# Kernel optimization log

Measured on AMD Instinct MI355X. Metric: run time of the kernel, lower is better.

## Reference

```python
import jax, jax.numpy as jnp
import numpy as np

TEMPERATURE = 8.0  # sqrt(head_dim=64)
NEG_INF = -1.0e9


def setup_inputs() -> dict:
    key = jax.random.key(0)
    kq, kk, kv, ks, km = jax.random.split(key, 5)
    B, H, S, D = 4, 8, 1024, 64
    q = jax.random.normal(kq, (B, H, S, D), dtype=jnp.float32)
    k = jax.random.normal(kk, (B, H, S, D), dtype=jnp.float32)
    v = jax.random.normal(kv, (B, H, S, D), dtype=jnp.float32)
    sph = jax.random.uniform(ks, (B, H, S, S), dtype=jnp.float32)
    mask = jax.random.randint(km, (B, 1, S, S), 0, 2, dtype=jnp.int32)
    return {"q": q, "k": k, "v": v, "sph": sph, "mask": mask}


def reference(q, k, v, sph, mask):
    # scores: [B,H,S,S]
    attn = jnp.einsum("bhqd,bhkd->bhqk", q / TEMPERATURE, k)
    attn = attn * sph
    attn = jnp.where(mask == 0, NEG_INF, attn)
    p_attn = jax.nn.softmax(attn, axis=-1)  # dropout in eval mode = identity
    output = jnp.einsum("bhqk,bhkd->bhqd", p_attn, v)
    return (output, p_attn)
```

## Files before the change

kernel.cpp:

```cpp
#include <hip/hip_runtime.h>

#define S_DIM 1024
#define D_DIM 64
#define TQ 16

typedef __attribute__((ext_vector_type(4))) float f32x4;
typedef __attribute__((ext_vector_type(4))) int i32x4;
typedef __attribute__((ext_vector_type(4))) unsigned short u16x4;
typedef __attribute__((ext_vector_type(8))) short short8;

__device__ inline unsigned short f2bf(float x) {
  unsigned int u = __builtin_bit_cast(unsigned int, x);
  u += 0x7fffu + ((u >> 16) & 1u);
  return (unsigned short)(u >> 16);
}

__device__ inline short8 pack8(f32x4 a, f32x4 b) {
  short8 r;
  r[0] = (short)f2bf(a.x); r[1] = (short)f2bf(a.y);
  r[2] = (short)f2bf(a.z); r[3] = (short)f2bf(a.w);
  r[4] = (short)f2bf(b.x); r[5] = (short)f2bf(b.y);
  r[6] = (short)f2bf(b.z); r[7] = (short)f2bf(b.w);
  return r;
}

__global__ __launch_bounds__(256, 3)
void sdpa_kernel(const float* __restrict__ qp, const float* __restrict__ kp,
                 const float* __restrict__ vp, const float* __restrict__ sphp,
                 const int* __restrict__ maskp,
                 float* __restrict__ outp, float* __restrict__ pp)
{
  __shared__ unsigned short pb[TQ][1032];
  __shared__ unsigned short vt[64][136];
  __shared__ float          red[2][4][16];

  const int tid   = threadIdx.x;
  const int lane  = tid & 63;
  const int wave  = tid >> 6;
  const int row16 = lane & 15;
  const int quad  = lane >> 4;

  const int bh = blockIdx.x >> 6;
  const int qt = blockIdx.x & 63;
  const int b  = bh >> 3;
  const int q0 = qt * TQ;

  const size_t bhS = (size_t)bh * S_DIM;

  const float* qrow = qp + (bhS + q0 + row16) * D_DIM + quad * 8;
  const f32x4 s8 = {0.125f, 0.125f, 0.125f, 0.125f};
  f32x4 qa = *(const f32x4*)(qrow);
  f32x4 qb = *(const f32x4*)(qrow + 4);
  f32x4 qc = *(const f32x4*)(qrow + 32);
  f32x4 qd = *(const f32x4*)(qrow + 36);
  const short8 bq0 = pack8(qa * s8, qb * s8);
  const short8 bq1 = pack8(qc * s8, qd * s8);

  const int kbase = wave * 256;
  f32x4 accs[16];
  #pragma unroll
  for (int t = 0; t < 16; ++t) {
    const float* krow = kp + (bhS + kbase + t * 16 + row16) * D_DIM + quad * 8;
    f32x4 ka = *(const f32x4*)(krow);
    f32x4 kb = *(const f32x4*)(krow + 4);
    f32x4 kc = *(const f32x4*)(krow + 32);
    f32x4 kd = *(const f32x4*)(krow + 36);
    f32x4 acc = {0.f, 0.f, 0.f, 0.f};
    acc = __builtin_amdgcn_mfma_f32_16x16x32_bf16(pack8(ka, kb), bq0, acc, 0, 0, 0);
    acc = __builtin_amdgcn_mfma_f32_16x16x32_bf16(pack8(kc, kd), bq1, acc, 0, 0, 0);
    accs[t] = acc;
  }

  const int q = q0 + row16;
  const float* sprow = sphp + (bhS + q) * S_DIM + kbase + quad * 4;
  const int*   mrow  = maskp + ((size_t)b * S_DIM + q) * S_DIM + kbase + quad * 4;

  float mx = -3.0e38f;
  #pragma unroll
  for (int t = 0; t < 16; ++t) {
    f32x4 p4 = *(const f32x4*)(sprow + t * 16);
    i32x4 m4 = *(const i32x4*)(mrow + t * 16);
    f32x4 s  = accs[t];
    s.x = (m4.x == 0) ? -1.0e9f : s.x * p4.x;
    s.y = (m4.y == 0) ? -1.0e9f : s.y * p4.y;
    s.z = (m4.z == 0) ? -1.0e9f : s.z * p4.z;
    s.w = (m4.w == 0) ? -1.0e9f : s.w * p4.w;
    accs[t] = s;
    mx = fmaxf(mx, fmaxf(fmaxf(s.x, s.y), fmaxf(s.z, s.w)));
  }
  mx = fmaxf(mx, __shfl_xor(mx, 16));
  mx = fmaxf(mx, __shfl_xor(mx, 32));
  if (quad == 0) red[0][wave][row16] = mx;
  __syncthreads();
  mx = fmaxf(fmaxf(red[0][0][row16], red[0][1][row16]),
             fmaxf(red[0][2][row16], red[0][3][row16]));

  float sum = 0.f;
  #pragma unroll
  for (int t = 0; t < 16; ++t) {
    f32x4 e;
    e.x = __expf(accs[t].x - mx);
    e.y = __expf(accs[t].y - mx);
    e.z = __expf(accs[t].z - mx);
    e.w = __expf(accs[t].w - mx);
    accs[t] = e;
    sum += (e.x + e.y) + (e.z + e.w);
  }
  sum += __shfl_xor(sum, 16);
  sum += __shfl_xor(sum, 32);
  if (quad == 0) red[1][wave][row16] = sum;
  __syncthreads();
  sum = (red[1][0][row16] + red[1][1][row16]) + (red[1][2][row16] + red[1][3][row16]);
  const float inv = 1.0f / sum;

  float* prow = pp + (bhS + q) * S_DIM + kbase + quad * 4;
  #pragma unroll
  for (int t = 0; t < 16; ++t) {
    f32x4 pv = accs[t] * inv;
    *(f32x4*)(prow + t * 16) = pv;
    u16x4 pbv;
    pbv.x = f2bf(pv.x); pbv.y = f2bf(pv.y);
    pbv.z = f2bf(pv.z); pbv.w = f2bf(pv.w);
    *(u16x4*)&pb[row16][kbase + t * 16 + quad * 4] = pbv;
  }

  f32x4 oacc = {0.f, 0.f, 0.f, 0.f};
  const float* vbase = vp + bhS * D_DIM;
  for (int vc = 0; vc < 8; ++vc) {
    __syncthreads();
    #pragma unroll
    for (int it = 0; it < 8; ++it) {
      const int i  = it * 256 + tid;
      const int c4 = i >> 7, rr = i & 127;
      f32x4 vv = *(const f32x4*)(vbase + (size_t)(vc * 128 + rr) * D_DIM + c4 * 4);
      vt[c4 * 4 + 0][rr] = f2bf(vv.x);
      vt[c4 * 4 + 1][rr] = f2bf(vv.y);
      vt[c4 * 4 + 2][rr] = f2bf(vv.z);
      vt[c4 * 4 + 3][rr] = f2bf(vv.w);
    }
    __syncthreads();
    #pragma unroll
    for (int kk = 0; kk < 4; ++kk) {
      short8 af = *(const short8*)&vt[wave * 16 + row16][kk * 32 + quad * 8];
      short8 bf = *(const short8*)&pb[row16][vc * 128 + kk * 32 + quad * 8];
      oacc = __builtin_amdgcn_mfma_f32_16x16x32_bf16(af, bf, oacc, 0, 0, 0);
    }
  }

  float* orow = outp + (bhS + q0 + row16) * D_DIM + wave * 16 + quad * 4;
  *(f32x4*)orow = oacc;
}

extern "C" void kernel_launch(void* const* d_in, const int* in_sizes, int n_in,
                              void* d_out, int out_size, void* d_ws, size_t ws_size,
                              hipStream_t stream) {
  const float* q    = (const float*)d_in[0];
  const float* k    = (const float*)d_in[1];
  const float* v    = (const float*)d_in[2];
  const float* sph  = (const float*)d_in[3];
  const int*   mask = (const int*)d_in[4];
  float* out  = (float*)d_out;
  float* patt = out + (size_t)4 * 8 * 1024 * 64;

  dim3 grid(32 * 64);
  dim3 block(256);
  hipLaunchKernelGGL(sdpa_kernel, grid, block, 0, stream,
                     q, k, v, sph, mask, out, patt);
}
```

Before: 390.9 us.

## Switch to fp16 MFMA and row-wise coalesced sph/mask/P access via LDS staging

Scores are staged in LDS as fp16 instead of being kept in registers, so each wave processes whole rows with contiguous 1 KB loads of sph and mask and contiguous stores of P. Previously each lane read and wrote 16-byte pieces strided across the key axis. Normalisation of the output is deferred to the end, and bf16 is replaced by fp16 with a -60000 mask sentinel. The main cost targeted is the poor coalescing of the large sph, mask and P streams. In exchange the kernel does extra LDS round trips and shuffle reductions per row, and fp16 storage of unnormalised scores loses some precision.

```diff
diff --git a/kernel.cpp b/kernel.cpp
--- a/kernel.cpp
+++ b/kernel.cpp
@@ -1,26 +1,19 @@
 #include <hip/hip_runtime.h>
 
 #define S_DIM 1024
-#define D_DIM 64
 #define TQ 16
 
 typedef __attribute__((ext_vector_type(4))) float f32x4;
 typedef __attribute__((ext_vector_type(4))) int i32x4;
-typedef __attribute__((ext_vector_type(4))) unsigned short u16x4;
-typedef __attribute__((ext_vector_type(8))) short short8;
+typedef _Float16 half4 __attribute__((ext_vector_type(4)));
+typedef _Float16 half8 __attribute__((ext_vector_type(8)));
 
-__device__ inline unsigned short f2bf(float x) {
-  unsigned int u = __builtin_bit_cast(unsigned int, x);
-  u += 0x7fffu + ((u >> 16) & 1u);
-  return (unsigned short)(u >> 16);
-}
-
-__device__ inline short8 pack8(f32x4 a, f32x4 b) {
-  short8 r;
-  r[0] = (short)f2bf(a.x); r[1] = (short)f2bf(a.y);
-  r[2] = (short)f2bf(a.z); r[3] = (short)f2bf(a.w);
-  r[4] = (short)f2bf(b.x); r[5] = (short)f2bf(b.y);
-  r[6] = (short)f2bf(b.z); r[7] = (short)f2bf(b.w);
+__device__ inline half8 pack8h(f32x4 a, f32x4 b) {
+  half8 r;
+  r[0] = (_Float16)a.x; r[1] = (_Float16)a.y;
+  r[2] = (_Float16)a.z; r[3] = (_Float16)a.w;
+  r[4] = (_Float16)b.x; r[5] = (_Float16)b.y;
+  r[6] = (_Float16)b.z; r[7] = (_Float16)b.w;
   return r;
 }
 
@@ -30,9 +23,9 @@
                  const int* __restrict__ maskp,
                  float* __restrict__ outp, float* __restrict__ pp)
 {
-  __shared__ unsigned short pb[TQ][1032];
-  __shared__ unsigned short vt[64][136];
-  __shared__ float          red[2][4][16];
+  __shared__ _Float16 pb[TQ][1032];
+  __shared__ _Float16 vt[64][136];
+  __shared__ float    red[2][4][16];
 
   const int tid   = threadIdx.x;
   const int lane  = tid & 63;
@@ -47,108 +40,116 @@
 
   const size_t bhS = (size_t)bh * S_DIM;
 
-  const float* qrow = qp + (bhS + q0 + row16) * D_DIM + quad * 8;
+  const float* qrow = qp + (bhS + q0 + row16) * 64 + quad * 8;
   const f32x4 s8 = {0.125f, 0.125f, 0.125f, 0.125f};
   f32x4 qa = *(const f32x4*)(qrow);
   f32x4 qb = *(const f32x4*)(qrow + 4);
   f32x4 qc = *(const f32x4*)(qrow + 32);
   f32x4 qd = *(const f32x4*)(qrow + 36);
-  const short8 bq0 = pack8(qa * s8, qb * s8);
-  const short8 bq1 = pack8(qc * s8, qd * s8);
+  const half8 bq0 = pack8h(qa * s8, qb * s8);
+  const half8 bq1 = pack8h(qc * s8, qd * s8);
 
   const int kbase = wave * 256;
-  f32x4 accs[16];
   #pragma unroll
   for (int t = 0; t < 16; ++t) {
-    const float* krow = kp + (bhS + kbase + t * 16 + row16) * D_DIM + quad * 8;
+    const float* krow = kp + (bhS + kbase + t * 16 + row16) * 64 + quad * 8;
     f32x4 ka = *(const f32x4*)(krow);
     f32x4 kb = *(const f32x4*)(krow + 4);
     f32x4 kc = *(const f32x4*)(krow + 32);
     f32x4 kd = *(const f32x4*)(krow + 36);
     f32x4 acc = {0.f, 0.f, 0.f, 0.f};
-    acc = __builtin_amdgcn_mfma_f32_16x16x32_bf16(pack8(ka, kb), bq0, acc, 0, 0, 0);
-    acc = __builtin_amdgcn_mfma_f32_16x16x32_bf16(pack8(kc, kd), bq1, acc, 0, 0, 0);
-    accs[t] = acc;
+    acc = __builtin_amdgcn_mfma_f32_16x16x32_f16(pack8h(ka, kb), bq0, acc, 0, 0, 0);
+    acc = __builtin_amdgcn_mfma_f32_16x16x32_f16(pack8h(kc, kd), bq1, acc, 0, 0, 0);
+    half4 hv; hv[0] = (_Float16)acc.x; hv[1] = (_Float16)acc.y;
+    hv[2] = (_Float16)acc.z; hv[3] = (_Float16)acc.w;
+    *(half4*)&pb[row16][kbase + t * 16 + quad * 4] = hv;
   }
+  __syncthreads();
 
-  const int q = q0 + row16;
-  const float* sprow = sphp + (bhS + q) * S_DIM + kbase + quad * 4;
-  const int*   mrow  = maskp + ((size_t)b * S_DIM + q) * S_DIM + kbase + quad * 4;
+  const int kcol = kbase + lane * 4;
 
-  float mx = -3.0e38f;
   #pragma unroll
-  for (int t = 0; t < 16; ++t) {
-    f32x4 p4 = *(const f32x4*)(sprow + t * 16);
-    i32x4 m4 = *(const i32x4*)(mrow + t * 16);
-    f32x4 s  = accs[t];
-    s.x = (m4.x == 0) ? -1.0e9f : s.x * p4.x;
-    s.y = (m4.y == 0) ? -1.0e9f : s.y * p4.y;
-    s.z = (m4.z == 0) ? -1.0e9f : s.z * p4.z;
-    s.w = (m4.w == 0) ? -1.0e9f : s.w * p4.w;
-    accs[t] = s;
-    mx = fmaxf(mx, fmaxf(fmaxf(s.x, s.y), fmaxf(s.z, s.w)));
+  for (int r = 0; r < TQ; ++r) {
+    const size_t rowoff = (bhS + q0 + r) * S_DIM + kcol;
+    f32x4 p4 = *(const f32x4*)(sphp + rowoff);
+    i32x4 m4 = *(const i32x4*)(maskp + (((size_t)b * S_DIM + q0 + r) * S_DIM + kcol));
+    half4 sh = *(half4*)&pb[r][kcol];
+    f32x4 ms;
+    ms.x = (m4.x == 0) ? -60000.f : (float)sh[0] * p4.x;
+    ms.y = (m4.y == 0) ? -60000.f : (float)sh[1] * p4.y;
+    ms.z = (m4.z == 0) ? -60000.f : (float)sh[2] * p4.z;
+    ms.w = (m4.w == 0) ? -60000.f : (float)sh[3] * p4.w;
+    half4 hv; hv[0] = (_Float16)ms.x; hv[1] = (_Float16)ms.y;
+    hv[2] = (_Float16)ms.z; hv[3] = (_Float16)ms.w;
+    *(half4*)&pb[r][kcol] = hv;
+    float mx = fmaxf(fmaxf(ms.x, ms.y), fmaxf(ms.z, ms.w));
+    #pragma unroll
+    for (int off = 32; off > 0; off >>= 1)
+      mx = fmaxf(mx, __shfl_xor(mx, off));
+    if (lane == 0) red[0][wave][r] = mx;
   }
-  mx = fmaxf(mx, __shfl_xor(mx, 16));
-  mx = fmaxf(mx, __shfl_xor(mx, 32));
-  if (quad == 0) red[0][wave][row16] = mx;
   __syncthreads();
-  mx = fmaxf(fmaxf(red[0][0][row16], red[0][1][row16]),
-             fmaxf(red[0][2][row16], red[0][3][row16]));
 
-  float sum = 0.f;
   #pragma unroll
-  for (int t = 0; t < 16; ++t) {
+  for (int r = 0; r < TQ; ++r) {
+    const float mx = fmaxf(fmaxf(red[0][0][r], red[0][1][r]),
+                           fmaxf(red[0][2][r], red[0][3][r]));
+    half4 sh = *(half4*)&pb[r][kcol];
     f32x4 e;
-    e.x = __expf(accs[t].x - mx);
-    e.y = __expf(accs[t].y - mx);
-    e.z = __expf(accs[t].z - mx);
-    e.w = __expf(accs[t].w - mx);
-    accs[t] = e;
-    sum += (e.x + e.y) + (e.z + e.w);
+    e.x = __expf((float)sh[0] - mx);
+    e.y = __expf((float)sh[1] - mx);
+    e.z = __expf((float)sh[2] - mx);
+    e.w = __expf((float)sh[3] - mx);
+    half4 hv; hv[0] = (_Float16)e.x; hv[1] = (_Float16)e.y;
+    hv[2] = (_Float16)e.z; hv[3] = (_Float16)e.w;
+    *(half4*)&pb[r][kcol] = hv;
+    float sum = (e.x + e.y) + (e.z + e.w);
+    #pragma unroll
+    for (int off = 32; off > 0; off >>= 1)
+      sum += __shfl_xor(sum, off);
+    if (lane == 0) red[1][wave][r] = sum;
   }
-  sum += __shfl_xor(sum, 16);
-  sum += __shfl_xor(sum, 32);
-  if (quad == 0) red[1][wave][row16] = sum;
   __syncthreads();
-  sum = (red[1][0][row16] + red[1][1][row16]) + (red[1][2][row16] + red[1][3][row16]);
-  const float inv = 1.0f / sum;
 
-  float* prow = pp + (bhS + q) * S_DIM + kbase + quad * 4;
   #pragma unroll
-  for (int t = 0; t < 16; ++t) {
-    f32x4 pv = accs[t] * inv;
-    *(f32x4*)(prow + t * 16) = pv;
-    u16x4 pbv;
-    pbv.x = f2bf(pv.x); pbv.y = f2bf(pv.y);
-    pbv.z = f2bf(pv.z); pbv.w = f2bf(pv.w);
-    *(u16x4*)&pb[row16][kbase + t * 16 + quad * 4] = pbv;
+  for (int r = 0; r < TQ; ++r) {
+    const float sum = (red[1][0][r] + red[1][1][r]) + (red[1][2][r] + red[1][3][r]);
+    const float inv = 1.0f / sum;
+    half4 e = *(half4*)&pb[r][kcol];
+    f32x4 pv;
+    pv.x = (float)e[0] * inv; pv.y = (float)e[1] * inv;
+    pv.z = (float)e[2] * inv; pv.w = (float)e[3] * inv;
+    *(f32x4*)(pp + (bhS + q0 + r) * S_DIM + kcol) = pv;
   }
 
   f32x4 oacc = {0.f, 0.f, 0.f, 0.f};
-  const float* vbase = vp + bhS * D_DIM;
+  const float* vbase = vp + bhS * 64;
   for (int vc = 0; vc < 8; ++vc) {
     __syncthreads();
     #pragma unroll
     for (int it = 0; it < 8; ++it) {
       const int i  = it * 256 + tid;
       const int c4 = i >> 7, rr = i & 127;
-      f32x4 vv = *(const f32x4*)(vbase + (size_t)(vc * 128 + rr) * D_DIM + c4 * 4);
-      vt[c4 * 4 + 0][rr] = f2bf(vv.x);
-      vt[c4 * 4 + 1][rr] = f2bf(vv.y);
-      vt[c4 * 4 + 2][rr] = f2bf(vv.z);
-      vt[c4 * 4 + 3][rr] = f2bf(vv.w);
+      f32x4 vv = *(const f32x4*)(vbase + (size_t)(vc * 128 + rr) * 64 + c4 * 4);
+      vt[c4 * 4 + 0][rr] = (_Float16)vv.x;
+      vt[c4 * 4 + 1][rr] = (_Float16)vv.y;
+      vt[c4 * 4 + 2][rr] = (_Float16)vv.z;
+      vt[c4 * 4 + 3][rr] = (_Float16)vv.w;
     }
     __syncthreads();
     #pragma unroll
     for (int kk = 0; kk < 4; ++kk) {
-      short8 af = *(const short8*)&vt[wave * 16 + row16][kk * 32 + quad * 8];
-      short8 bf = *(const short8*)&pb[row16][vc * 128 + kk * 32 + quad * 8];
-      oacc = __builtin_amdgcn_mfma_f32_16x16x32_bf16(af, bf, oacc, 0, 0, 0);
+      half8 af = *(half8*)&vt[wave * 16 + row16][kk * 32 + quad * 8];
+      half8 bf = *(half8*)&pb[row16][vc * 128 + kk * 32 + quad * 8];
+      oacc = __builtin_amdgcn_mfma_f32_16x16x32_f16(af, bf, oacc, 0, 0, 0);
     }
   }
 
-  float* orow = outp + (bhS + q0 + row16) * D_DIM + wave * 16 + quad * 4;
-  *(f32x4*)orow = oacc;
+  const float ssum = (red[1][0][row16] + red[1][1][row16]) +
+                     (red[1][2][row16] + red[1][3][row16]);
+  const float invq = 1.0f / ssum;
+  float* orow = outp + (bhS + q0 + row16) * 64 + wave * 16 + quad * 4;
+  *(f32x4*)orow = oacc * invq;
 }
 
 extern "C" void kernel_launch(void* const* d_in, const int* in_sizes, int n_in,
```

Measured after the change: 384.5 us. Within noise of the previous version (-1.6%).
